# Performance work log

Measured on AMD Instinct MI355X. Metric: run time of the kernel, lower is better.

## Reference

```python
import jax, jax.numpy as jnp
import numpy as np

N, B, F = 10000, 2, 64
NAS = 64
OUT = 64


def setup_inputs() -> dict:
    key = jax.random.key(0)
    k1, k2, k3, k4 = jax.random.split(key, 4)
    x = jax.random.normal(k1, (N, B, F), dtype=jnp.float32)
    dists_max = jax.random.uniform(k2, (N, NAS), dtype=jnp.float32)
    dists_argmax = jax.random.randint(k3, (N, NAS), 0, N)
    # xavier-uniform-ish init for linear_hidden: W [OUT, 2F], b [OUT]
    gain = float(np.sqrt(2.0))  # calculate_gain('relu')
    bound = gain * float(np.sqrt(6.0 / (2 * F + OUT)))
    W_hidden = jax.random.uniform(k4, (OUT, 2 * F), dtype=jnp.float32,
                                  minval=-bound, maxval=bound)
    b_hidden = jnp.zeros((OUT,), dtype=jnp.float32)
    return {"x": x, "dists_max": dists_max, "dists_argmax": dists_argmax,
            "W_hidden": W_hidden, "b_hidden": b_hidden}


def reference(x, dists_max, dists_argmax, W_hidden, b_hidden):
    # x: [N, B, F] -> [B, N, F]
    xb = jnp.transpose(x, (1, 0, 2))
    # anchor-set gather: [B, N, NAS, F], scaled by inverse-distance score
    anchor = xb[:, dists_argmax, :] * dists_max[None, :, :, None]
    # concat([anchor, source]) @ W^T split into two matmuls;
    # source part is independent of NAS so compute it once and broadcast.
    Wa, Ws = W_hidden[:, :F], W_hidden[:, F:]  # each [OUT, F]
    src_term = jnp.einsum('bnf,of->bno', xb, Ws)  # [B, N, OUT]
    msg = jnp.einsum('bnaf,of->bnao', anchor, Wa) + src_term[:, :, None, :] + b_hidden
    # mean over anchor sets (last_layer_flag=False path), dropout p=0 -> identity
    out = msg.mean(axis=2)  # [B, N, OUT]
    return jnp.transpose(out, (1, 0, 2))  # [N, B, OUT]
```

## Files before the change

### kernel.cpp

```cpp
#include <hip/hip_runtime.h>

#define NN   10000
#define NASD 64
#define FD   64
#define OD   64

__launch_bounds__(256, 4)
__global__ void pgnn_kernel(const float* __restrict__ x,
                            const float* __restrict__ dmax,
                            const int*   __restrict__ amax,
                            const float* __restrict__ W,
                            const float* __restrict__ bias,
                            float*       __restrict__ out,
                            int nWavesTotal) {
    __shared__ float Wlds[OD * 129];
    __shared__ float blds[OD];
    __shared__ float ulds[4][256];

    const int tid  = threadIdx.x;
    const int lane = tid & 63;
    const int w    = tid >> 6;

    for (int j = tid; j < OD * 128; j += 256) {
        int o = j >> 7, k = j & 127;
        Wlds[o * 129 + k] = W[j];
    }
    if (tid < OD) blds[tid] = bias[tid];
    __syncthreads();

    float* u = ulds[w];
    const int e0 = lane * 2, e1 = lane * 2 + 1;

    for (int n = blockIdx.x * 4 + w; n < NN; n += nWavesTotal) {
        float dv = dmax[n * 64 + lane];
        int   iv = amax[n * 64 + lane];
        float g0 = 0.f, g1 = 0.f;
        #pragma unroll 8
        for (int a = 0; a < 64; ++a) {
            int   mm = __builtin_amdgcn_readlane(iv, a);
            float dd = __uint_as_float(__builtin_amdgcn_readlane(__float_as_uint(dv), a));
            const float2 xv = *reinterpret_cast<const float2*>(x + mm * 128 + e0);
            g0 = fmaf(dd, xv.x, g0);
            g1 = fmaf(dd, xv.y, g1);
        }
        g0 *= (1.0f / 64.0f);
        g1 *= (1.0f / 64.0f);

        u[(e0 & 63) * 2 + (e0 >> 6)] = g0;
        u[(e1 & 63) * 2 + (e1 >> 6)] = g1;
        const float2 xs = *reinterpret_cast<const float2*>(x + n * 128 + e0);
        u[(64 + (e0 & 63)) * 2 + (e0 >> 6)] = xs.x;
        u[(64 + (e1 & 63)) * 2 + (e1 >> 6)] = xs.y;

        asm volatile("s_waitcnt lgkmcnt(0)" ::: "memory");
        __builtin_amdgcn_sched_barrier(0);

        float acc0 = blds[lane];
        float acc1 = acc0;
        const float* wrow = &Wlds[lane * 129];
        #pragma unroll 4
        for (int k = 0; k < 128; k += 2) {
            float4 uu = *reinterpret_cast<const float4*>(&u[k * 2]);
            float w0 = wrow[k], w1 = wrow[k + 1];
            acc0 = fmaf(uu.x, w0, acc0);
            acc1 = fmaf(uu.y, w0, acc1);
            acc0 = fmaf(uu.z, w1, acc0);
            acc1 = fmaf(uu.w, w1, acc1);
        }
        out[n * 128 + lane]      = acc0;
        out[n * 128 + 64 + lane] = acc1;

        asm volatile("s_waitcnt lgkmcnt(0)" ::: "memory");
        __builtin_amdgcn_sched_barrier(0);
    }
}

extern "C" void kernel_launch(void* const* d_in, const int* in_sizes, int n_in,
                              void* d_out, int out_size, void* d_ws, size_t ws_size,
                              hipStream_t stream) {
    const float* x    = (const float*)d_in[0];
    const float* dmax = (const float*)d_in[1];
    const int*   amax = (const int*)  d_in[2];
    const float* W    = (const float*)d_in[3];
    const float* bias = (const float*)d_in[4];
    float* out = (float*)d_out;

    const int blocks = 1024;
    pgnn_kernel<<<blocks, 256, 0, stream>>>(x, dmax, amax, W, bias, out, blocks * 4);
}
```

Before: 93.75 us.

## Project x through W first, then gather bf16 projected rows

```diff
diff --git a/kernel.cpp b/kernel.cpp
--- a/kernel.cpp
+++ b/kernel.cpp
@@ -1,90 +1,104 @@
 #include <hip/hip_runtime.h>
 
-#define NN   10000
-#define NASD 64
-#define FD   64
-#define OD   64
+#define NODES 10000
+#define ROWS  20000
+
+__launch_bounds__(256, 2)
+__global__ void pgnn_proj(const float* __restrict__ x,
+                          const float* __restrict__ W,
+                          const float* __restrict__ bias,
+                          unsigned short* __restrict__ Yb,
+                          float* __restrict__ S,
+                          int nWaves) {
+    const int lane = threadIdx.x & 63;
+    const int wid  = (blockIdx.x * blockDim.x + threadIdx.x) >> 6;
+
+    float wreg[128];
+    {
+        const float4* wr = reinterpret_cast<const float4*>(W + lane * 128);
+        #pragma unroll
+        for (int q = 0; q < 32; ++q) {
+            float4 v = wr[q];
+            wreg[q * 4 + 0] = v.x; wreg[q * 4 + 1] = v.y;
+            wreg[q * 4 + 2] = v.z; wreg[q * 4 + 3] = v.w;
+        }
+    }
+    const float bl = bias[lane];
+
+    int r = wid;
+    if (r >= ROWS) return;
+    float xv = x[r * 64 + lane];
+    while (true) {
+        const int rn = r + nWaves;
+        float xnext = 0.f;
+        if (rn < ROWS) xnext = x[rn * 64 + lane];
+
+        float acc0 = 0.f, acc1 = bl;
+        #pragma unroll
+        for (int k = 0; k < 64; ++k) {
+            float sx = __uint_as_float(
+                __builtin_amdgcn_readlane(__float_as_uint(xv), k));
+            acc0 = fmaf(sx, wreg[k],      acc0);
+            acc1 = fmaf(sx, wreg[64 + k], acc1);
+        }
+        unsigned u = __float_as_uint(acc0);
+        u += 0x7FFFu + ((u >> 16) & 1u);
+        Yb[r * 64 + lane] = (unsigned short)(u >> 16);
+        S [r * 64 + lane] = acc1;
+
+        if (rn >= ROWS) break;
+        r = rn; xv = xnext;
+    }
+}
 
 __launch_bounds__(256, 4)
-__global__ void pgnn_kernel(const float* __restrict__ x,
-                            const float* __restrict__ dmax,
+__global__ void pgnn_gather(const float* __restrict__ dmax,
                             const int*   __restrict__ amax,
-                            const float* __restrict__ W,
-                            const float* __restrict__ bias,
-                            float*       __restrict__ out,
-                            int nWavesTotal) {
-    __shared__ float Wlds[OD * 129];
-    __shared__ float blds[OD];
-    __shared__ float ulds[4][256];
+                            const unsigned short* __restrict__ Yb,
+                            const float* __restrict__ S,
+                            float*       __restrict__ out) {
+    const int lane = threadIdx.x & 63;
+    const int n    = (blockIdx.x * blockDim.x + threadIdx.x) >> 6;
+    if (n >= NODES) return;
 
-    const int tid  = threadIdx.x;
-    const int lane = tid & 63;
-    const int w    = tid >> 6;
+    const float dv = dmax[n * 64 + lane];
+    const int   iv = amax[n * 64 + lane];
 
-    for (int j = tid; j < OD * 128; j += 256) {
-        int o = j >> 7, k = j & 127;
-        Wlds[o * 129 + k] = W[j];
+    float a0 = 0.f, a1 = 0.f;
+    #pragma unroll 16
+    for (int a = 0; a < 64; ++a) {
+        const int   m  = __builtin_amdgcn_readlane(iv, a);
+        const float dd = __uint_as_float(
+            __builtin_amdgcn_readlane(__float_as_uint(dv), a));
+        const unsigned yv =
+            *reinterpret_cast<const unsigned*>(Yb + m * 128 + lane * 2);
+        a0 = fmaf(dd, __uint_as_float(yv << 16),          a0);
+        a1 = fmaf(dd, __uint_as_float(yv & 0xFFFF0000u), a1);
     }
-    if (tid < OD) blds[tid] = bias[tid];
-    __syncthreads();
 
-    float* u = ulds[w];
-    const int e0 = lane * 2, e1 = lane * 2 + 1;
-
-    for (int n = blockIdx.x * 4 + w; n < NN; n += nWavesTotal) {
-        float dv = dmax[n * 64 + lane];
-        int   iv = amax[n * 64 + lane];
-        float g0 = 0.f, g1 = 0.f;
-        #pragma unroll 8
-        for (int a = 0; a < 64; ++a) {
-            int   mm = __builtin_amdgcn_readlane(iv, a);
-            float dd = __uint_as_float(__builtin_amdgcn_readlane(__float_as_uint(dv), a));
-            const float2 xv = *reinterpret_cast<const float2*>(x + mm * 128 + e0);
-            g0 = fmaf(dd, xv.x, g0);
-            g1 = fmaf(dd, xv.y, g1);
-        }
-        g0 *= (1.0f / 64.0f);
-        g1 *= (1.0f / 64.0f);
-
-        u[(e0 & 63) * 2 + (e0 >> 6)] = g0;
-        u[(e1 & 63) * 2 + (e1 >> 6)] = g1;
-        const float2 xs = *reinterpret_cast<const float2*>(x + n * 128 + e0);
-        u[(64 + (e0 & 63)) * 2 + (e0 >> 6)] = xs.x;
-        u[(64 + (e1 & 63)) * 2 + (e1 >> 6)] = xs.y;
-
-        asm volatile("s_waitcnt lgkmcnt(0)" ::: "memory");
-        __builtin_amdgcn_sched_barrier(0);
-
-        float acc0 = blds[lane];
-        float acc1 = acc0;
-        const float* wrow = &Wlds[lane * 129];
-        #pragma unroll 4
-        for (int k = 0; k < 128; k += 2) {
-            float4 uu = *reinterpret_cast<const float4*>(&u[k * 2]);
-            float w0 = wrow[k], w1 = wrow[k + 1];
-            acc0 = fmaf(uu.x, w0, acc0);
-            acc1 = fmaf(uu.y, w0, acc1);
-            acc0 = fmaf(uu.z, w1, acc0);
-            acc1 = fmaf(uu.w, w1, acc1);
-        }
-        out[n * 128 + lane]      = acc0;
-        out[n * 128 + 64 + lane] = acc1;
-
-        asm volatile("s_waitcnt lgkmcnt(0)" ::: "memory");
-        __builtin_amdgcn_sched_barrier(0);
-    }
+    const float2 sv = *reinterpret_cast<const float2*>(S + n * 128 + lane * 2);
+    float2 o2;
+    o2.x = a0 * (1.0f / 64.0f) + sv.x;
+    o2.y = a1 * (1.0f / 64.0f) + sv.y;
+    *reinterpret_cast<float2*>(out + n * 128 + lane * 2) = o2;
 }
 
 extern "C" void kernel_launch(void* const* d_in, const int* in_sizes, int n_in,
                               void* d_out, int out_size, void* d_ws, size_t ws_size,
                               hipStream_t stream) {
     const float* x    = (const float*)d_in[0];
-    const float* dmax = (const float*)d_in[1];
-    const int*   amax = (const int*)  d_in[2];
+    const float* dm   = (const float*)d_in[1];
+    const int*   am   = (const int*)  d_in[2];
     const float* W    = (const float*)d_in[3];
     const float* bias = (const float*)d_in[4];
     float* out = (float*)d_out;
 
-    const int blocks = 1024;
-    pgnn_kernel<<<blocks, 256, 0, stream>>>(x, dmax, amax, W, bias, out, blocks * 4);
+    unsigned short* Yb = (unsigned short*)d_ws;
+    float*          S  = (float*)((char*)d_ws + (4u << 20));
+
+    const int projBlocks = 320;
+    pgnn_proj<<<projBlocks, 256, 0, stream>>>(x, W, bias, Yb, S, projBlocks * 4);
+
+    const int gatherBlocks = (NODES + 3) / 4;
+    pgnn_gather<<<gatherBlocks, 256, 0, stream>>>(dm, am, Yb, S, out);
 }
```

New measurement: 100.4 us. 7.1% more time.
